# Kernel optimization log

Measured on AMD Instinct MI355X. Metric: run time of the kernel, lower is better.

The kernel has to match this reference:

```python
import jax, jax.numpy as jnp
import numpy as np

B, S, D = 8, 2048, 768
SCALE = jnp.sqrt(jnp.float32(D))


def setup_inputs() -> dict:
    key = jax.random.key(0)
    ks = jax.random.split(key, 9)
    sd = 1.0 / np.sqrt(D)
    return {
        "x": jax.random.normal(ks[0], (B, S, D), jnp.float32),
        "Wq": jax.random.normal(ks[1], (D, D), jnp.float32) * sd,
        "bq": jax.random.normal(ks[2], (D,), jnp.float32) * sd,
        "Wk": jax.random.normal(ks[3], (D, D), jnp.float32) * sd,
        "bk": jax.random.normal(ks[4], (D,), jnp.float32) * sd,
        "Wv": jax.random.normal(ks[5], (D, D), jnp.float32) * sd,
        "bv": jax.random.normal(ks[6], (D,), jnp.float32) * sd,
        "Wp": jax.random.normal(ks[7], (D, D), jnp.float32) * sd,
        "bp": jax.random.normal(ks[8], (D,), jnp.float32) * sd,
    }


def reference(x, Wq, bq, Wk, bk, Wv, bv, Wp, bp):
    # Linear layers: y = x @ W^T + b (torch nn.Linear convention)
    Q = jnp.einsum("bsd,ed->bse", x, Wq) + bq
    K = jnp.einsum("bsd,ed->bse", x, Wk) + bk
    V = jnp.einsum("bsd,ed->bse", x, Wv) + bv
    # Full attention matrix (no head split in original module)
    alpha = jnp.einsum("bqd,bkd->bqk", Q, K) / SCALE  # [B,S,S]
    alpha = jax.nn.softmax(alpha, axis=-1)
    # dropout is identity in eval mode
    out = jnp.einsum("bqk,bkd->bqd", alpha, V)
    out = jnp.einsum("bsd,ed->bse", out, Wp) + bp
    return out
```

## Files before the change

kernel.cpp:

```cpp
#include <hip/hip_runtime.h>
#include <stdint.h>


typedef __attribute__((ext_vector_type(8))) short short8;
typedef __attribute__((ext_vector_type(4))) float f32x4;

typedef const __attribute__((address_space(1))) void gvoid_t;
typedef __attribute__((address_space(3))) void lvoid_t;

__device__ __forceinline__ float b2f(unsigned short u) {
  union { unsigned int u; float f; } v;
  v.u = ((unsigned int)u) << 16;
  return v.f;
}
__device__ __forceinline__ unsigned short f2b(float f) {
  union { float f; unsigned int u; } v; v.f = f;
  unsigned int u = v.u;
  return (unsigned short)((u + 0x7fffu + ((u >> 16) & 1u)) >> 16);
}

__global__ void detect_dtype(const unsigned int* __restrict__ xu, int* __restrict__ flagp) {
  __shared__ int red[256];
  const int t = threadIdx.x;
  int cnt = 0;
  for (int i = t; i < 4096; i += 256) {
    unsigned int u = xu[i];
    float v = fabsf(b2f((unsigned short)(u & 0xffffu)));
    cnt += (v >= 0.125f && v <= 8.0f) ? 1 : 0;
  }
  red[t] = cnt;
  __syncthreads();
#pragma unroll
  for (int o = 128; o > 0; o >>= 1) {
    if (t < o) red[t] += red[t + o];
    __syncthreads();
  }
  if (t == 0) flagp[0] = (red[0] > 2048) ? 1 : 0;
}

struct Cvt9 {
  const void* s[9];
  unsigned short* d[9];
  long long n8[9];
  long long total8;
};

__global__ __launch_bounds__(256) void convert_inputs(Cvt9 C, const int* __restrict__ flagp) {
  if (flagp[0] != 0) return;
  long long g = (long long)blockIdx.x * 256 + threadIdx.x;
  if (g >= C.total8) return;
  int s = 0;
  long long off = g;
  while (off >= C.n8[s]) { off -= C.n8[s]; ++s; }
  const float* sf = (const float*)C.s[s] + off * 8;
  unsigned short* dp = C.d[s] + off * 8;
  float4 a = ((const float4*)sf)[0];
  float4 b = ((const float4*)sf)[1];
  uint4 o;
  o.x = (unsigned int)f2b(a.x) | ((unsigned int)f2b(a.y) << 16);
  o.y = (unsigned int)f2b(a.z) | ((unsigned int)f2b(a.w) << 16);
  o.z = (unsigned int)f2b(b.x) | ((unsigned int)f2b(b.y) << 16);
  o.w = (unsigned int)f2b(b.z) | ((unsigned int)f2b(b.w) << 16);
  *(uint4*)dp = o;
}

__device__ __forceinline__ void gemm_core(
    const unsigned short* __restrict__ Ab, const unsigned short* __restrict__ Bb,
    int lda, int ldb, int K, int m0, int n0,
    unsigned short* As, unsigned short* Bs, f32x4 (&acc)[4][4])
{
  const int t    = threadIdx.x;
  const int w    = t >> 6;
  const int lane = t & 63;
  const int lo   = lane & 15;
  const int quad = lane >> 4;
  const int wr   = w >> 1;
  const int wc   = w & 1;
  const int srow  = t >> 2;
  const int skoff = (t & 3) * 8;

  for (int k0 = 0; k0 < K; k0 += 64) {
#pragma unroll
    for (int c = 0; c < 2; ++c) {
#pragma unroll
      for (int r = 0; r < 2; ++r) {
        const unsigned short* ga = Ab + (size_t)(m0 + r * 64 + srow) * lda + (k0 + c * 32 + skoff);
        __builtin_amdgcn_global_load_lds((gvoid_t*)ga, (lvoid_t*)(As + c * 4096 + r * 2048 + w * 512), 16, 0, 0);
        const unsigned short* gb = Bb + (size_t)(n0 + r * 64 + srow) * ldb + (k0 + c * 32 + skoff);
        __builtin_amdgcn_global_load_lds((gvoid_t*)gb, (lvoid_t*)(Bs + c * 4096 + r * 2048 + w * 512), 16, 0, 0);
      }
    }
    __syncthreads();

#pragma unroll
    for (int c = 0; c < 2; ++c) {
      short8 af[4], bf[4];
#pragma unroll
      for (int i = 0; i < 4; ++i)
        af[i] = *(const short8*)(As + c * 4096 + (wr * 64 + i * 16 + lo) * 32 + quad * 8);
#pragma unroll
      for (int j = 0; j < 4; ++j)
        bf[j] = *(const short8*)(Bs + c * 4096 + (wc * 64 + j * 16 + lo) * 32 + quad * 8);

#pragma unroll
      for (int i = 0; i < 4; ++i)
#pragma unroll
        for (int j = 0; j < 4; ++j)
          acc[i][j] = __builtin_amdgcn_mfma_f32_16x16x32_bf16(af[i], bf[j], acc[i][j], 0, 0, 0);
    }
    __syncthreads();
  }
}

__device__ __forceinline__ void tile_to_lds(
    unsigned short* Ls, f32x4 (&acc)[4][4], int mode,
    const unsigned short* bias_n0, const float* rlrow, float scale)
{
  const int t = threadIdx.x;
  const int w = t >> 6, lane = t & 63;
  const int lo = lane & 15, quad = lane >> 4, wr = w >> 1, wc = w & 1;
#pragma unroll
  for (int j = 0; j < 4; ++j) {
    const int ct = wc * 64 + j * 16 + lo;
    const float bv = (mode == 0) ? b2f(bias_n0[ct]) : 0.f;
#pragma unroll
    for (int i = 0; i < 4; ++i) {
      const int rt = wr * 64 + i * 16 + quad * 4;
#pragma unroll
      for (int r = 0; r < 4; ++r) {
        float v = acc[i][j][r];
        if (mode == 0)      v += bv;
        else if (mode == 2) v = __expf(fminf(v * scale, 30.f));
        else                v *= rlrow[rt + r];
        Ls[(rt + r) * 136 + ct] = f2b(v);
      }
    }
  }
  __syncthreads();
}

__device__ __forceinline__ void lds_to_global_bf16(
    const unsigned short* Ls, unsigned short* Cg, int ldc)
{
  const int t = threadIdx.x;
  const int cr = t >> 4, cc = (t & 15) * 8;
#pragma unroll
  for (int r0 = 0; r0 < 128; r0 += 16) {
    uint4 v = *(const uint4*)(Ls + (r0 + cr) * 136 + cc);
    *(uint4*)(Cg + (size_t)(r0 + cr) * ldc + cc) = v;
  }
}

__global__ __launch_bounds__(256, 2) void qkv_k(
    const unsigned short* __restrict__ x0, const unsigned short* __restrict__ x1,
    const unsigned short* __restrict__ Wq0, const unsigned short* __restrict__ Wq1,
    const unsigned short* __restrict__ bq0, const unsigned short* __restrict__ bq1,
    const unsigned short* __restrict__ Wk0, const unsigned short* __restrict__ Wk1,
    const unsigned short* __restrict__ bk0, const unsigned short* __restrict__ bk1,
    const unsigned short* __restrict__ Wv0, const unsigned short* __restrict__ Wv1,
    const unsigned short* __restrict__ bv0, const unsigned short* __restrict__ bv1,
    unsigned short* __restrict__ qb, unsigned short* __restrict__ kb,
    unsigned short* __restrict__ vt, const int* __restrict__ flagp)
{
  __shared__ unsigned short smem[17408];
  const int flg = flagp[0];
  const int sel = blockIdx.y / 6;
  const int n0  = (blockIdx.y % 6) * 128;
  const int m0  = blockIdx.x * 128;

  const unsigned short* A = flg ? x0 : x1;
  const unsigned short* W;
  const unsigned short* bi;
  if (sel == 0)      { W = flg ? Wq0 : Wq1; bi = flg ? bq0 : bq1; }
  else if (sel == 1) { W = flg ? Wk0 : Wk1; bi = flg ? bk0 : bk1; }
  else               { W = flg ? Wv0 : Wv1; bi = flg ? bv0 : bv1; }

  f32x4 acc[4][4] = {};
  gemm_core(A, W, 768, 768, 768, m0, n0, smem, smem + 8192, acc);

  const int t = threadIdx.x;
  const int w = t >> 6, lane = t & 63;
  const int lo = lane & 15, quad = lane >> 4, wr = w >> 1, wc = w & 1;

  if (sel < 2) {
    tile_to_lds(smem, acc, 0, bi + n0, nullptr, 0.f);
    unsigned short* dst = (sel == 0) ? qb : kb;
    lds_to_global_bf16(smem, dst + (size_t)m0 * 768 + n0, 768);
    return;
  }

  unsigned short* Ls = smem;
#pragma unroll
  for (int i = 0; i < 4; ++i) {
    const int rt = wr * 64 + i * 16 + quad * 4;
#pragma unroll
    for (int j = 0; j < 4; ++j) {
      const int ct = wc * 64 + j * 16 + lo;
      const float bvv = b2f(bi[n0 + ct]);
      ushort4 pk;
      pk.x = f2b(acc[i][j][0] + bvv);
      pk.y = f2b(acc[i][j][1] + bvv);
      pk.z = f2b(acc[i][j][2] + bvv);
      pk.w = f2b(acc[i][j][3] + bvv);
      *(ushort4*)(Ls + ct * 136 + rt) = pk;
    }
  }
  __syncthreads();
  const int bb  = m0 >> 11;
  const int sin = m0 & 2047;
  unsigned short* Cb = vt + (size_t)bb * (768 * 2048);
#pragma unroll
  for (int e0 = 0; e0 < 128; e0 += 16) {
    const int et = e0 + (t >> 4);
    const int st = (t & 15) * 8;
    uint4 val = *(const uint4*)(Ls + et * 136 + st);
    *(uint4*)(Cb + (size_t)(n0 + et) * 2048 + (sin + st)) = val;
  }
}

__global__ __launch_bounds__(256, 2) void score_k(
    const unsigned short* __restrict__ Q, const unsigned short* __restrict__ Kb,
    unsigned short* __restrict__ E, float* __restrict__ rl, float scale)
{
  __shared__ unsigned short smem[17408];
  const int m0 = blockIdx.x * 128, n0 = blockIdx.y * 128, bz = blockIdx.z;

  f32x4 acc[4][4] = {};
  gemm_core(Q + (size_t)bz * 1572864, Kb + (size_t)bz * 1572864,
            768, 768, 768, m0, n0, smem, smem + 8192, acc);

  tile_to_lds(smem, acc, 2, nullptr, nullptr, scale);
  lds_to_global_bf16(smem, E + (size_t)bz * 4194304 + (size_t)m0 * 2048 + n0, 2048);

  const int t = threadIdx.x;
  const int row = t >> 1, half = t & 1;
  const unsigned short* lr = smem + row * 136 + half * 64;
  float s = 0.f;
#pragma unroll
  for (int q8 = 0; q8 < 8; ++q8) {
    uint4 v = *(const uint4*)(lr + q8 * 8);
    unsigned int uu[4] = {v.x, v.y, v.z, v.w};
#pragma unroll
    for (int c = 0; c < 4; ++c)
      s += b2f((unsigned short)(uu[c] & 0xffffu)) + b2f((unsigned short)(uu[c] >> 16));
  }
  s += __shfl_xor(s, 1);
  if (half == 0) atomicAdd(rl + bz * 2048 + m0 + row, s);
}

__global__ __launch_bounds__(256) void inv_k(float* __restrict__ rl) {
  const int i = blockIdx.x * 256 + threadIdx.x;
  if (i < 16384) rl[i] = 1.0f / fmaxf(rl[i], 1e-30f);
}

__global__ __launch_bounds__(256, 2) void pv_k(
    const unsigned short* __restrict__ E, const unsigned short* __restrict__ Vt,
    const float* __restrict__ rl, unsigned short* __restrict__ attn)
{
  __shared__ unsigned short smem[17408];
  const int m0 = blockIdx.x * 128, n0 = blockIdx.y * 128, bz = blockIdx.z;

  f32x4 acc[4][4] = {};
  gemm_core(E + (size_t)bz * 4194304, Vt + (size_t)bz * 1572864,
            2048, 2048, 2048, m0, n0, smem, smem + 8192, acc);

  tile_to_lds(smem, acc, 3, nullptr, rl + bz * 2048 + m0, 0.f);
  lds_to_global_bf16(smem, attn + (size_t)bz * 1572864 + (size_t)m0 * 768 + n0, 768);
}

__global__ __launch_bounds__(256, 2) void out_k(
    const unsigned short* __restrict__ attn,
    const unsigned short* __restrict__ Wp0, const unsigned short* __restrict__ Wp1,
    const unsigned short* __restrict__ bp0, const unsigned short* __restrict__ bp1,
    void* __restrict__ outp, const int* __restrict__ flagp)
{
  __shared__ unsigned short smem[17408];
  const int flg = flagp[0];
  const int m0 = blockIdx.x * 128, n0 = blockIdx.y * 128;
  const unsigned short* W  = flg ? Wp0 : Wp1;
  const unsigned short* bi = flg ? bp0 : bp1;

  f32x4 acc[4][4] = {};
  gemm_core(attn, W, 768, 768, 768, m0, n0, smem, smem + 8192, acc);

  if (flg) {
    tile_to_lds(smem, acc, 0, bi + n0, nullptr, 0.f);
    lds_to_global_bf16(smem, (unsigned short*)outp + (size_t)m0 * 768 + n0, 768);
    return;
  }

  const int t = threadIdx.x;
  const int w = t >> 6, lane = t & 63;
  const int lo = lane & 15, quad = lane >> 4, wr = w >> 1, wc = w & 1;
  float* Lf = (float*)smem;
  float* Of = (float*)outp;
#pragma unroll
  for (int h = 0; h < 2; ++h) {
    __syncthreads();
    if (wc == h) {
#pragma unroll
      for (int j = 0; j < 4; ++j) {
        const int cl = j * 16 + lo;
        const float bvv = b2f(bi[n0 + h * 64 + cl]);
#pragma unroll
        for (int i = 0; i < 4; ++i) {
          const int rt = wr * 64 + i * 16 + quad * 4;
#pragma unroll
          for (int r = 0; r < 4; ++r)
            Lf[(rt + r) * 68 + cl] = acc[i][j][r] + bvv;
        }
      }
    }
    __syncthreads();
    const int cr = t >> 4, cc = (t & 15) * 4;
#pragma unroll
    for (int r0 = 0; r0 < 128; r0 += 16) {
      float4 v = *(const float4*)(Lf + (r0 + cr) * 68 + cc);
      *(float4*)(Of + (size_t)(m0 + r0 + cr) * 768 + n0 + h * 64 + cc) = v;
    }
  }
}

extern "C" void kernel_launch(void* const* d_in, const int* in_sizes, int n_in,
                              void* d_out, int out_size, void* d_ws, size_t ws_size,
                              hipStream_t stream) {
  (void)in_sizes; (void)n_in; (void)out_size; (void)ws_size;
  const unsigned short* x  = (const unsigned short*)d_in[0];
  const unsigned short* Wq = (const unsigned short*)d_in[1];
  const unsigned short* bq = (const unsigned short*)d_in[2];
  const unsigned short* Wk = (const unsigned short*)d_in[3];
  const unsigned short* bk = (const unsigned short*)d_in[4];
  const unsigned short* Wv = (const unsigned short*)d_in[5];
  const unsigned short* bv = (const unsigned short*)d_in[6];
  const unsigned short* Wp = (const unsigned short*)d_in[7];
  const unsigned short* bp = (const unsigned short*)d_in[8];

  char* ws = (char*)d_ws;
  int*   flagp = (int*)ws;
  float* rl    = (float*)(ws + 4096);
  unsigned short* wcv = (unsigned short*)(ws + ((size_t)1 << 20));
  unsigned short* qb  = (unsigned short*)(ws + ((size_t)8  << 20));
  unsigned short* kb  = (unsigned short*)(ws + ((size_t)32 << 20));
  unsigned short* vt  = (unsigned short*)(ws + ((size_t)56 << 20));
  unsigned short* eb  = (unsigned short*)(ws + ((size_t)80 << 20));
  unsigned short* xb  = eb;
  unsigned short* attn = qb;

  unsigned short* wqb = wcv;
  unsigned short* bqb = wcv + 589824;
  unsigned short* wkb = wcv + 590592;
  unsigned short* bkb = wcv + 1180416;
  unsigned short* wvb = wcv + 1181184;
  unsigned short* bvb = wcv + 1771008;
  unsigned short* wpb = wcv + 1771776;
  unsigned short* bpb = wcv + 2361600;

  const float inv_scale = 0.036084391824351615f;
  dim3 blk(256);

  detect_dtype<<<1, 256, 0, stream>>>((const unsigned int*)d_in[0], flagp);

  Cvt9 cv;
  cv.s[0] = d_in[0]; cv.d[0] = xb;  cv.n8[0] = 12582912 / 8;
  cv.s[1] = d_in[1]; cv.d[1] = wqb; cv.n8[1] = 589824 / 8;
  cv.s[2] = d_in[2]; cv.d[2] = bqb; cv.n8[2] = 768 / 8;
  cv.s[3] = d_in[3]; cv.d[3] = wkb; cv.n8[3] = 589824 / 8;
  cv.s[4] = d_in[4]; cv.d[4] = bkb; cv.n8[4] = 768 / 8;
  cv.s[5] = d_in[5]; cv.d[5] = wvb; cv.n8[5] = 589824 / 8;
  cv.s[6] = d_in[6]; cv.d[6] = bvb; cv.n8[6] = 768 / 8;
  cv.s[7] = d_in[7]; cv.d[7] = wpb; cv.n8[7] = 589824 / 8;
  cv.s[8] = d_in[8]; cv.d[8] = bpb; cv.n8[8] = 768 / 8;
  cv.total8 = (12582912 + 4 * (589824 + 768)) / 8;
  convert_inputs<<<(unsigned)((cv.total8 + 255) / 256), blk, 0, stream>>>(cv, flagp);

  hipMemsetAsync(rl, 0, 16384 * sizeof(float), stream);

  qkv_k<<<dim3(128, 18, 1), blk, 0, stream>>>(
      x, xb, Wq, wqb, bq, bqb, Wk, wkb, bk, bkb, Wv, wvb, bv, bvb,
      qb, kb, vt, flagp);

  score_k<<<dim3(16, 16, 8), blk, 0, stream>>>(qb, kb, eb, rl, inv_scale);

  inv_k<<<64, blk, 0, stream>>>(rl);

  pv_k<<<dim3(16, 6, 8), blk, 0, stream>>>(eb, vt, rl, attn);

  out_k<<<dim3(128, 6, 1), blk, 0, stream>>>(attn, Wp, wpb, bp, bpb, d_out, flagp);
}
```

Baseline: 371.7 us.

## Switch GEMMs to 32x32x16 MFMA, drop dtype detection and inverse kernel

Replaces the 16x16x32 bf16 MFMA tiling with 32x32x16 MFMA (2x2 accumulators of 16 floats per wave) in the shared GEMM core and in all epilogues. The runtime dtype-detection kernel and the bf16-input fast path are removed, so inputs are always assumed fp32 and always converted. The separate row-sum reciprocal kernel is folded into the PV epilogue using a hardware rcp. Fewer launches and larger MFMA tiles aim to cut issue overhead and LDS reads per FLOP. The rcp approximation is slightly less accurate than a true division.

```diff
diff --git a/kernel.cpp b/kernel.cpp
--- a/kernel.cpp
+++ b/kernel.cpp
@@ -3,7 +3,7 @@
 
 
 typedef __attribute__((ext_vector_type(8))) short short8;
-typedef __attribute__((ext_vector_type(4))) float f32x4;
+typedef __attribute__((ext_vector_type(16))) float f32x16;
 
 typedef const __attribute__((address_space(1))) void gvoid_t;
 typedef __attribute__((address_space(3))) void lvoid_t;
@@ -17,25 +17,6 @@
   union { float f; unsigned int u; } v; v.f = f;
   unsigned int u = v.u;
   return (unsigned short)((u + 0x7fffu + ((u >> 16) & 1u)) >> 16);
-}
-
-__global__ void detect_dtype(const unsigned int* __restrict__ xu, int* __restrict__ flagp) {
-  __shared__ int red[256];
-  const int t = threadIdx.x;
-  int cnt = 0;
-  for (int i = t; i < 4096; i += 256) {
-    unsigned int u = xu[i];
-    float v = fabsf(b2f((unsigned short)(u & 0xffffu)));
-    cnt += (v >= 0.125f && v <= 8.0f) ? 1 : 0;
-  }
-  red[t] = cnt;
-  __syncthreads();
-#pragma unroll
-  for (int o = 128; o > 0; o >>= 1) {
-    if (t < o) red[t] += red[t + o];
-    __syncthreads();
-  }
-  if (t == 0) flagp[0] = (red[0] > 2048) ? 1 : 0;
 }
 
 struct Cvt9 {
@@ -45,8 +26,7 @@
   long long total8;
 };
 
-__global__ __launch_bounds__(256) void convert_inputs(Cvt9 C, const int* __restrict__ flagp) {
-  if (flagp[0] != 0) return;
+__global__ __launch_bounds__(256) void convert_inputs(Cvt9 C) {
   long long g = (long long)blockIdx.x * 256 + threadIdx.x;
   if (g >= C.total8) return;
   int s = 0;
@@ -67,13 +47,13 @@
 __device__ __forceinline__ void gemm_core(
     const unsigned short* __restrict__ Ab, const unsigned short* __restrict__ Bb,
     int lda, int ldb, int K, int m0, int n0,
-    unsigned short* As, unsigned short* Bs, f32x4 (&acc)[4][4])
+    unsigned short* As, unsigned short* Bs, f32x16 (&acc)[2][2])
 {
   const int t    = threadIdx.x;
   const int w    = t >> 6;
   const int lane = t & 63;
-  const int lo   = lane & 15;
-  const int quad = lane >> 4;
+  const int l32  = lane & 31;
+  const int kh8  = (lane >> 5) * 8;
   const int wr   = w >> 1;
   const int wc   = w & 1;
   const int srow  = t >> 2;
@@ -94,45 +74,52 @@
 
 #pragma unroll
     for (int c = 0; c < 2; ++c) {
-      short8 af[4], bf[4];
-#pragma unroll
-      for (int i = 0; i < 4; ++i)
-        af[i] = *(const short8*)(As + c * 4096 + (wr * 64 + i * 16 + lo) * 32 + quad * 8);
-#pragma unroll
-      for (int j = 0; j < 4; ++j)
-        bf[j] = *(const short8*)(Bs + c * 4096 + (wc * 64 + j * 16 + lo) * 32 + quad * 8);
-
-#pragma unroll
-      for (int i = 0; i < 4; ++i)
-#pragma unroll
-        for (int j = 0; j < 4; ++j)
-          acc[i][j] = __builtin_amdgcn_mfma_f32_16x16x32_bf16(af[i], bf[j], acc[i][j], 0, 0, 0);
+#pragma unroll
+      for (int h = 0; h < 2; ++h) {
+        short8 af[2], bf[2];
+#pragma unroll
+        for (int i = 0; i < 2; ++i)
+          af[i] = *(const short8*)(As + c * 4096 + (wr * 64 + i * 32 + l32) * 32 + h * 16 + kh8);
+#pragma unroll
+        for (int j = 0; j < 2; ++j)
+          bf[j] = *(const short8*)(Bs + c * 4096 + (wc * 64 + j * 32 + l32) * 32 + h * 16 + kh8);
+
+#pragma unroll
+        for (int i = 0; i < 2; ++i)
+#pragma unroll
+          for (int j = 0; j < 2; ++j)
+            acc[i][j] = __builtin_amdgcn_mfma_f32_32x32x16_bf16(af[i], bf[j], acc[i][j], 0, 0, 0);
+      }
     }
     __syncthreads();
   }
 }
 
 __device__ __forceinline__ void tile_to_lds(
-    unsigned short* Ls, f32x4 (&acc)[4][4], int mode,
+    unsigned short* Ls, f32x16 (&acc)[2][2], int mode,
     const unsigned short* bias_n0, const float* rlrow, float scale)
 {
   const int t = threadIdx.x;
   const int w = t >> 6, lane = t & 63;
-  const int lo = lane & 15, quad = lane >> 4, wr = w >> 1, wc = w & 1;
-#pragma unroll
-  for (int j = 0; j < 4; ++j) {
-    const int ct = wc * 64 + j * 16 + lo;
+  const int l32 = lane & 31, wr = w >> 1, wc = w & 1;
+  const int r4 = (lane >> 5) * 4;
+#pragma unroll
+  for (int j = 0; j < 2; ++j) {
+    const int ct = wc * 64 + j * 32 + l32;
     const float bv = (mode == 0) ? b2f(bias_n0[ct]) : 0.f;
 #pragma unroll
-    for (int i = 0; i < 4; ++i) {
-      const int rt = wr * 64 + i * 16 + quad * 4;
-#pragma unroll
-      for (int r = 0; r < 4; ++r) {
-        float v = acc[i][j][r];
-        if (mode == 0)      v += bv;
-        else if (mode == 2) v = __expf(fminf(v * scale, 30.f));
-        else                v *= rlrow[rt + r];
-        Ls[(rt + r) * 136 + ct] = f2b(v);
+    for (int i = 0; i < 2; ++i) {
+#pragma unroll
+      for (int g = 0; g < 4; ++g) {
+        const int rbase = wr * 64 + i * 32 + g * 8 + r4;
+#pragma unroll
+        for (int r = 0; r < 4; ++r) {
+          float v = acc[i][j][g * 4 + r];
+          if (mode == 0)      v += bv;
+          else if (mode == 2) v = __expf(fminf(v * scale, 30.f));
+          else                v *= __builtin_amdgcn_rcpf(rlrow[rbase + r]);
+          Ls[(rbase + r) * 136 + ct] = f2b(v);
+        }
       }
     }
   }
@@ -152,35 +139,31 @@
 }
 
 __global__ __launch_bounds__(256, 2) void qkv_k(
-    const unsigned short* __restrict__ x0, const unsigned short* __restrict__ x1,
-    const unsigned short* __restrict__ Wq0, const unsigned short* __restrict__ Wq1,
-    const unsigned short* __restrict__ bq0, const unsigned short* __restrict__ bq1,
-    const unsigned short* __restrict__ Wk0, const unsigned short* __restrict__ Wk1,
-    const unsigned short* __restrict__ bk0, const unsigned short* __restrict__ bk1,
-    const unsigned short* __restrict__ Wv0, const unsigned short* __restrict__ Wv1,
-    const unsigned short* __restrict__ bv0, const unsigned short* __restrict__ bv1,
+    const unsigned short* __restrict__ xb,
+    const unsigned short* __restrict__ Wq, const unsigned short* __restrict__ bq,
+    const unsigned short* __restrict__ Wk, const unsigned short* __restrict__ bk,
+    const unsigned short* __restrict__ Wv, const unsigned short* __restrict__ bv,
     unsigned short* __restrict__ qb, unsigned short* __restrict__ kb,
-    unsigned short* __restrict__ vt, const int* __restrict__ flagp)
+    unsigned short* __restrict__ vt)
 {
   __shared__ unsigned short smem[17408];
-  const int flg = flagp[0];
   const int sel = blockIdx.y / 6;
   const int n0  = (blockIdx.y % 6) * 128;
   const int m0  = blockIdx.x * 128;
 
-  const unsigned short* A = flg ? x0 : x1;
   const unsigned short* W;
   const unsigned short* bi;
-  if (sel == 0)      { W = flg ? Wq0 : Wq1; bi = flg ? bq0 : bq1; }
-  else if (sel == 1) { W = flg ? Wk0 : Wk1; bi = flg ? bk0 : bk1; }
-  else               { W = flg ? Wv0 : Wv1; bi = flg ? bv0 : bv1; }
-
-  f32x4 acc[4][4] = {};
-  gemm_core(A, W, 768, 768, 768, m0, n0, smem, smem + 8192, acc);
+  if (sel == 0)      { W = Wq; bi = bq; }
+  else if (sel == 1) { W = Wk; bi = bk; }
+  else               { W = Wv; bi = bv; }
+
+  f32x16 acc[2][2] = {};
+  gemm_core(xb, W, 768, 768, 768, m0, n0, smem, smem + 8192, acc);
 
   const int t = threadIdx.x;
   const int w = t >> 6, lane = t & 63;
-  const int lo = lane & 15, quad = lane >> 4, wr = w >> 1, wc = w & 1;
+  const int l32 = lane & 31, wr = w >> 1, wc = w & 1;
+  const int r4 = (lane >> 5) * 4;
 
   if (sel < 2) {
     tile_to_lds(smem, acc, 0, bi + n0, nullptr, 0.f);
@@ -191,18 +174,21 @@
 
   unsigned short* Ls = smem;
 #pragma unroll
-  for (int i = 0; i < 4; ++i) {
-    const int rt = wr * 64 + i * 16 + quad * 4;
-#pragma unroll
-    for (int j = 0; j < 4; ++j) {
-      const int ct = wc * 64 + j * 16 + lo;
-      const float bvv = b2f(bi[n0 + ct]);
-      ushort4 pk;
-      pk.x = f2b(acc[i][j][0] + bvv);
-      pk.y = f2b(acc[i][j][1] + bvv);
-      pk.z = f2b(acc[i][j][2] + bvv);
-      pk.w = f2b(acc[i][j][3] + bvv);
-      *(ushort4*)(Ls + ct * 136 + rt) = pk;
+  for (int j = 0; j < 2; ++j) {
+    const int ct = wc * 64 + j * 32 + l32;
+    const float bvv = b2f(bi[n0 + ct]);
+#pragma unroll
+    for (int i = 0; i < 2; ++i) {
+#pragma unroll
+      for (int g = 0; g < 4; ++g) {
+        const int rbase = wr * 64 + i * 32 + g * 8 + r4;
+        ushort4 pk;
+        pk.x = f2b(acc[i][j][g * 4 + 0] + bvv);
+        pk.y = f2b(acc[i][j][g * 4 + 1] + bvv);
+        pk.z = f2b(acc[i][j][g * 4 + 2] + bvv);
+        pk.w = f2b(acc[i][j][g * 4 + 3] + bvv);
+        *(ushort4*)(Ls + ct * 136 + rbase) = pk;
+      }
     }
   }
   __syncthreads();
@@ -225,7 +211,7 @@
   __shared__ unsigned short smem[17408];
   const int m0 = blockIdx.x * 128, n0 = blockIdx.y * 128, bz = blockIdx.z;
 
-  f32x4 acc[4][4] = {};
+  f32x16 acc[2][2] = {};
   gemm_core(Q + (size_t)bz * 1572864, Kb + (size_t)bz * 1572864,
             768, 768, 768, m0, n0, smem, smem + 8192, acc);
 
@@ -248,11 +234,6 @@
   if (half == 0) atomicAdd(rl + bz * 2048 + m0 + row, s);
 }
 
-__global__ __launch_bounds__(256) void inv_k(float* __restrict__ rl) {
-  const int i = blockIdx.x * 256 + threadIdx.x;
-  if (i < 16384) rl[i] = 1.0f / fmaxf(rl[i], 1e-30f);
-}
-
 __global__ __launch_bounds__(256, 2) void pv_k(
     const unsigned short* __restrict__ E, const unsigned short* __restrict__ Vt,
     const float* __restrict__ rl, unsigned short* __restrict__ attn)
@@ -260,7 +241,7 @@
   __shared__ unsigned short smem[17408];
   const int m0 = blockIdx.x * 128, n0 = blockIdx.y * 128, bz = blockIdx.z;
 
-  f32x4 acc[4][4] = {};
+  f32x16 acc[2][2] = {};
   gemm_core(E + (size_t)bz * 4194304, Vt + (size_t)bz * 1572864,
             2048, 2048, 2048, m0, n0, smem, smem + 8192, acc);
 
@@ -270,44 +251,37 @@
 
 __global__ __launch_bounds__(256, 2) void out_k(
     const unsigned short* __restrict__ attn,
-    const unsigned short* __restrict__ Wp0, const unsigned short* __restrict__ Wp1,
-    const unsigned short* __restrict__ bp0, const unsigned short* __restrict__ bp1,
-    void* __restrict__ outp, const int* __restrict__ flagp)
+    const unsigned short* __restrict__ Wp, const unsigned short* __restrict__ bp,
+    float* __restrict__ Of)
 {
   __shared__ unsigned short smem[17408];
-  const int flg = flagp[0];
   const int m0 = blockIdx.x * 128, n0 = blockIdx.y * 128;
-  const unsigned short* W  = flg ? Wp0 : Wp1;
-  const unsigned short* bi = flg ? bp0 : bp1;
-
-  f32x4 acc[4][4] = {};
-  gemm_core(attn, W, 768, 768, 768, m0, n0, smem, smem + 8192, acc);
-
-  if (flg) {
-    tile_to_lds(smem, acc, 0, bi + n0, nullptr, 0.f);
-    lds_to_global_bf16(smem, (unsigned short*)outp + (size_t)m0 * 768 + n0, 768);
-    return;
-  }
+
+  f32x16 acc[2][2] = {};
+  gemm_core(attn, Wp, 768, 768, 768, m0, n0, smem, smem + 8192, acc);
 
   const int t = threadIdx.x;
   const int w = t >> 6, lane = t & 63;
-  const int lo = lane & 15, quad = lane >> 4, wr = w >> 1, wc = w & 1;
+  const int l32 = lane & 31, wr = w >> 1, wc = w & 1;
+  const int r4 = (lane >> 5) * 4;
   float* Lf = (float*)smem;
-  float* Of = (float*)outp;
 #pragma unroll
   for (int h = 0; h < 2; ++h) {
     __syncthreads();
     if (wc == h) {
 #pragma unroll
-      for (int j = 0; j < 4; ++j) {
-        const int cl = j * 16 + lo;
-        const float bvv = b2f(bi[n0 + h * 64 + cl]);
-#pragma unroll
-        for (int i = 0; i < 4; ++i) {
-          const int rt = wr * 64 + i * 16 + quad * 4;
-#pragma unroll
-          for (int r = 0; r < 4; ++r)
-            Lf[(rt + r) * 68 + cl] = acc[i][j][r] + bvv;
+      for (int j = 0; j < 2; ++j) {
+        const int cl = j * 32 + l32;
+        const float bvv = b2f(bp[n0 + h * 64 + cl]);
+#pragma unroll
+        for (int i = 0; i < 2; ++i) {
+#pragma unroll
+          for (int g = 0; g < 4; ++g) {
+            const int rbase = wr * 64 + i * 32 + g * 8 + r4;
+#pragma unroll
+            for (int r = 0; r < 4; ++r)
+              Lf[(rbase + r) * 68 + cl] = acc[i][j][g * 4 + r] + bvv;
+          }
         }
       }
     }
@@ -325,18 +299,8 @@
                               void* d_out, int out_size, void* d_ws, size_t ws_size,
                               hipStream_t stream) {
   (void)in_sizes; (void)n_in; (void)out_size; (void)ws_size;
-  const unsigned short* x  = (const unsigned short*)d_in[0];
-  const unsigned short* Wq = (const unsigned short*)d_in[1];
-  const unsigned short* bq = (const unsigned short*)d_in[2];
-  const unsigned short* Wk = (const unsigned short*)d_in[3];
-  const unsigned short* bk = (const unsigned short*)d_in[4];
-  const unsigned short* Wv = (const unsigned short*)d_in[5];
-  const unsigned short* bv = (const unsigned short*)d_in[6];
-  const unsigned short* Wp = (const unsigned short*)d_in[7];
-  const unsigned short* bp = (const unsigned short*)d_in[8];
 
   char* ws = (char*)d_ws;
-  int*   flagp = (int*)ws;
   float* rl    = (float*)(ws + 4096);
   unsigned short* wcv = (unsigned short*)(ws + ((size_t)1 << 20));
   unsigned short* qb  = (unsigned short*)(ws + ((size_t)8  << 20));
@@ -357,8 +321,6 @@
 
   const float inv_scale = 0.036084391824351615f;
   dim3 blk(256);
-
-  detect_dtype<<<1, 256, 0, stream>>>((const unsigned int*)d_in[0], flagp);
 
   Cvt9 cv;
   cv.s[0] = d_in[0]; cv.d[0] = xb;  cv.n8[0] = 12582912 / 8;
@@ -371,19 +333,15 @@
   cv.s[7] = d_in[7]; cv.d[7] = wpb; cv.n8[7] = 589824 / 8;
   cv.s[8] = d_in[8]; cv.d[8] = bpb; cv.n8[8] = 768 / 8;
   cv.total8 = (12582912 + 4 * (589824 + 768)) / 8;
-  convert_inputs<<<(unsigned)((cv.total8 + 255) / 256), blk, 0, stream>>>(cv, flagp);
+  convert_inputs<<<(unsigned)((cv.total8 + 255) / 256), blk, 0, stream>>>(cv);
 
   hipMemsetAsync(rl, 0, 16384 * sizeof(float), stream);
 
-  qkv_k<<<dim3(128, 18, 1), blk, 0, stream>>>(
-      x, xb, Wq, wqb, bq, bqb, Wk, wkb, bk, bkb, Wv, wvb, bv, bvb,
-      qb, kb, vt, flagp);
+  qkv_k<<<dim3(128, 18, 1), blk, 0, stream>>>(xb, wqb, bqb, wkb, bkb, wvb, bvb, qb, kb, vt);
 
   score_k<<<dim3(16, 16, 8), blk, 0, stream>>>(qb, kb, eb, rl, inv_scale);
 
-  inv_k<<<64, blk, 0, stream>>>(rl);
-
   pv_k<<<dim3(16, 6, 8), blk, 0, stream>>>(eb, vt, rl, attn);
 
-  out_k<<<dim3(128, 6, 1), blk, 0, stream>>>(attn, Wp, wpb, bp, bpb, d_out, flagp);
-}
+  out_k<<<dim3(128, 6, 1), blk, 0, stream>>>(attn, wpb, bpb, (float*)d_out);
+}
```

New measurement: 373.3 us. About the same (+0.4%).

## Swizzle GEMM LDS layout, drop dtype detection and fold inverse into epilogue

Applied to the files above, without the earlier changes.

Removes the runtime bf16/fp32 dtype detection kernel and all flag branches, so inputs are always treated as fp32 and converted. Applies an XOR-style rotation to the k-offset used when staging tiles into LDS and when reading them back, to avoid LDS bank conflicts in the MFMA fragment loads. Removes the separate reciprocal kernel by applying a hardware rcp of the row sum inside the PV epilogue. This saves two small launches, but the rcp no longer clamps the row sum with a small minimum as the old kernel did.

```diff
diff --git a/kernel.cpp b/kernel.cpp
--- a/kernel.cpp
+++ b/kernel.cpp
@@ -17,25 +17,6 @@
   union { float f; unsigned int u; } v; v.f = f;
   unsigned int u = v.u;
   return (unsigned short)((u + 0x7fffu + ((u >> 16) & 1u)) >> 16);
-}
-
-__global__ void detect_dtype(const unsigned int* __restrict__ xu, int* __restrict__ flagp) {
-  __shared__ int red[256];
-  const int t = threadIdx.x;
-  int cnt = 0;
-  for (int i = t; i < 4096; i += 256) {
-    unsigned int u = xu[i];
-    float v = fabsf(b2f((unsigned short)(u & 0xffffu)));
-    cnt += (v >= 0.125f && v <= 8.0f) ? 1 : 0;
-  }
-  red[t] = cnt;
-  __syncthreads();
-#pragma unroll
-  for (int o = 128; o > 0; o >>= 1) {
-    if (t < o) red[t] += red[t + o];
-    __syncthreads();
-  }
-  if (t == 0) flagp[0] = (red[0] > 2048) ? 1 : 0;
 }
 
 struct Cvt9 {
@@ -45,8 +26,7 @@
   long long total8;
 };
 
-__global__ __launch_bounds__(256) void convert_inputs(Cvt9 C, const int* __restrict__ flagp) {
-  if (flagp[0] != 0) return;
+__global__ __launch_bounds__(256) void convert_inputs(Cvt9 C) {
   long long g = (long long)blockIdx.x * 256 + threadIdx.x;
   if (g >= C.total8) return;
   int s = 0;
@@ -77,7 +57,9 @@
   const int wr   = w >> 1;
   const int wc   = w & 1;
   const int srow  = t >> 2;
-  const int skoff = (t & 3) * 8;
+  const int sq    = ((t & 3) - ((t >> 3) & 3)) & 3;
+  const int skoff = sq * 8;
+  const int rq    = ((quad + (lo >> 1)) & 3) * 8;
 
   for (int k0 = 0; k0 < K; k0 += 64) {
 #pragma unroll
@@ -97,10 +79,10 @@
       short8 af[4], bf[4];
 #pragma unroll
       for (int i = 0; i < 4; ++i)
-        af[i] = *(const short8*)(As + c * 4096 + (wr * 64 + i * 16 + lo) * 32 + quad * 8);
+        af[i] = *(const short8*)(As + c * 4096 + wr * 2048 + (i * 16 + lo) * 32 + rq);
 #pragma unroll
       for (int j = 0; j < 4; ++j)
-        bf[j] = *(const short8*)(Bs + c * 4096 + (wc * 64 + j * 16 + lo) * 32 + quad * 8);
+        bf[j] = *(const short8*)(Bs + c * 4096 + wc * 2048 + (j * 16 + lo) * 32 + rq);
 
 #pragma unroll
       for (int i = 0; i < 4; ++i)
@@ -131,7 +113,7 @@
         float v = acc[i][j][r];
         if (mode == 0)      v += bv;
         else if (mode == 2) v = __expf(fminf(v * scale, 30.f));
-        else                v *= rlrow[rt + r];
+        else                v *= __builtin_amdgcn_rcpf(rlrow[rt + r]);
         Ls[(rt + r) * 136 + ct] = f2b(v);
       }
     }
@@ -152,31 +134,26 @@
 }
 
 __global__ __launch_bounds__(256, 2) void qkv_k(
-    const unsigned short* __restrict__ x0, const unsigned short* __restrict__ x1,
-    const unsigned short* __restrict__ Wq0, const unsigned short* __restrict__ Wq1,
-    const unsigned short* __restrict__ bq0, const unsigned short* __restrict__ bq1,
-    const unsigned short* __restrict__ Wk0, const unsigned short* __restrict__ Wk1,
-    const unsigned short* __restrict__ bk0, const unsigned short* __restrict__ bk1,
-    const unsigned short* __restrict__ Wv0, const unsigned short* __restrict__ Wv1,
-    const unsigned short* __restrict__ bv0, const unsigned short* __restrict__ bv1,
+    const unsigned short* __restrict__ xb,
+    const unsigned short* __restrict__ Wq, const unsigned short* __restrict__ bq,
+    const unsigned short* __restrict__ Wk, const unsigned short* __restrict__ bk,
+    const unsigned short* __restrict__ Wv, const unsigned short* __restrict__ bv,
     unsigned short* __restrict__ qb, unsigned short* __restrict__ kb,
-    unsigned short* __restrict__ vt, const int* __restrict__ flagp)
+    unsigned short* __restrict__ vt)
 {
   __shared__ unsigned short smem[17408];
-  const int flg = flagp[0];
   const int sel = blockIdx.y / 6;
   const int n0  = (blockIdx.y % 6) * 128;
   const int m0  = blockIdx.x * 128;
 
-  const unsigned short* A = flg ? x0 : x1;
   const unsigned short* W;
   const unsigned short* bi;
-  if (sel == 0)      { W = flg ? Wq0 : Wq1; bi = flg ? bq0 : bq1; }
-  else if (sel == 1) { W = flg ? Wk0 : Wk1; bi = flg ? bk0 : bk1; }
-  else               { W = flg ? Wv0 : Wv1; bi = flg ? bv0 : bv1; }
+  if (sel == 0)      { W = Wq; bi = bq; }
+  else if (sel == 1) { W = Wk; bi = bk; }
+  else               { W = Wv; bi = bv; }
 
   f32x4 acc[4][4] = {};
-  gemm_core(A, W, 768, 768, 768, m0, n0, smem, smem + 8192, acc);
+  gemm_core(xb, W, 768, 768, 768, m0, n0, smem, smem + 8192, acc);
 
   const int t = threadIdx.x;
   const int w = t >> 6, lane = t & 63;
@@ -248,11 +225,6 @@
   if (half == 0) atomicAdd(rl + bz * 2048 + m0 + row, s);
 }
 
-__global__ __launch_bounds__(256) void inv_k(float* __restrict__ rl) {
-  const int i = blockIdx.x * 256 + threadIdx.x;
-  if (i < 16384) rl[i] = 1.0f / fmaxf(rl[i], 1e-30f);
-}
-
 __global__ __launch_bounds__(256, 2) void pv_k(
     const unsigned short* __restrict__ E, const unsigned short* __restrict__ Vt,
     const float* __restrict__ rl, unsigned short* __restrict__ attn)
@@ -270,30 +242,19 @@
 
 __global__ __launch_bounds__(256, 2) void out_k(
     const unsigned short* __restrict__ attn,
-    const unsigned short* __restrict__ Wp0, const unsigned short* __restrict__ Wp1,
-    const unsigned short* __restrict__ bp0, const unsigned short* __restrict__ bp1,
-    void* __restrict__ outp, const int* __restrict__ flagp)
+    const unsigned short* __restrict__ Wp, const unsigned short* __restrict__ bp,
+    float* __restrict__ Of)
 {
   __shared__ unsigned short smem[17408];
-  const int flg = flagp[0];
   const int m0 = blockIdx.x * 128, n0 = blockIdx.y * 128;
-  const unsigned short* W  = flg ? Wp0 : Wp1;
-  const unsigned short* bi = flg ? bp0 : bp1;
 
   f32x4 acc[4][4] = {};
-  gemm_core(attn, W, 768, 768, 768, m0, n0, smem, smem + 8192, acc);
-
-  if (flg) {
-    tile_to_lds(smem, acc, 0, bi + n0, nullptr, 0.f);
-    lds_to_global_bf16(smem, (unsigned short*)outp + (size_t)m0 * 768 + n0, 768);
-    return;
-  }
+  gemm_core(attn, Wp, 768, 768, 768, m0, n0, smem, smem + 8192, acc);
 
   const int t = threadIdx.x;
   const int w = t >> 6, lane = t & 63;
   const int lo = lane & 15, quad = lane >> 4, wr = w >> 1, wc = w & 1;
   float* Lf = (float*)smem;
-  float* Of = (float*)outp;
 #pragma unroll
   for (int h = 0; h < 2; ++h) {
     __syncthreads();
@@ -301,7 +262,7 @@
 #pragma unroll
       for (int j = 0; j < 4; ++j) {
         const int cl = j * 16 + lo;
-        const float bvv = b2f(bi[n0 + h * 64 + cl]);
+        const float bvv = b2f(bp[n0 + h * 64 + cl]);
 #pragma unroll
         for (int i = 0; i < 4; ++i) {
           const int rt = wr * 64 + i * 16 + quad * 4;
@@ -325,18 +286,8 @@
                               void* d_out, int out_size, void* d_ws, size_t ws_size,
                               hipStream_t stream) {
   (void)in_sizes; (void)n_in; (void)out_size; (void)ws_size;
-  const unsigned short* x  = (const unsigned short*)d_in[0];
-  const unsigned short* Wq = (const unsigned short*)d_in[1];
-  const unsigned short* bq = (const unsigned short*)d_in[2];
-  const unsigned short* Wk = (const unsigned short*)d_in[3];
-  const unsigned short* bk = (const unsigned short*)d_in[4];
-  const unsigned short* Wv = (const unsigned short*)d_in[5];
-  const unsigned short* bv = (const unsigned short*)d_in[6];
-  const unsigned short* Wp = (const unsigned short*)d_in[7];
-  const unsigned short* bp = (const unsigned short*)d_in[8];
 
   char* ws = (char*)d_ws;
-  int*   flagp = (int*)ws;
   float* rl    = (float*)(ws + 4096);
   unsigned short* wcv = (unsigned short*)(ws + ((size_t)1 << 20));
   unsigned short* qb  = (unsigned short*)(ws + ((size_t)8  << 20));
@@ -357,8 +308,6 @@
 
   const float inv_scale = 0.036084391824351615f;
   dim3 blk(256);
-
-  detect_dtype<<<1, 256, 0, stream>>>((const unsigned int*)d_in[0], flagp);
 
   Cvt9 cv;
   cv.s[0] = d_in[0]; cv.d[0] = xb;  cv.n8[0] = 12582912 / 8;
@@ -371,19 +320,15 @@
   cv.s[7] = d_in[7]; cv.d[7] = wpb; cv.n8[7] = 589824 / 8;
   cv.s[8] = d_in[8]; cv.d[8] = bpb; cv.n8[8] = 768 / 8;
   cv.total8 = (12582912 + 4 * (589824 + 768)) / 8;
-  convert_inputs<<<(unsigned)((cv.total8 + 255) / 256), blk, 0, stream>>>(cv, flagp);
+  convert_inputs<<<(unsigned)((cv.total8 + 255) / 256), blk, 0, stream>>>(cv);
 
   hipMemsetAsync(rl, 0, 16384 * sizeof(float), stream);
 
-  qkv_k<<<dim3(128, 18, 1), blk, 0, stream>>>(
-      x, xb, Wq, wqb, bq, bqb, Wk, wkb, bk, bkb, Wv, wvb, bv, bvb,
-      qb, kb, vt, flagp);
+  qkv_k<<<dim3(128, 18, 1), blk, 0, stream>>>(xb, wqb, bqb, wkb, bkb, wvb, bvb, qb, kb, vt);
 
   score_k<<<dim3(16, 16, 8), blk, 0, stream>>>(qb, kb, eb, rl, inv_scale);
 
-  inv_k<<<64, blk, 0, stream>>>(rl);
-
   pv_k<<<dim3(16, 6, 8), blk, 0, stream>>>(eb, vt, rl, attn);
 
-  out_k<<<dim3(128, 6, 1), blk, 0, stream>>>(attn, Wp, wpb, bp, bpb, d_out, flagp);
-}
+  out_k<<<dim3(128, 6, 1), blk, 0, stream>>>(attn, wpb, bpb, (float*)d_out);
+}
```

Result: faster. 362.6 us (-2.4%).
